# Kernel optimization log

Hardware: AMD Instinct MI355X
Metric: run time of the kernel (lower is better)

## Reference

```python
import jax, jax.numpy as jnp
import numpy as np

N = 100_000   # nodes
E = 1_600_000 # edges
F = 16        # input node features
H = 32        # embedding_size
B = 256       # graphs in batch


def setup_inputs() -> dict:
    key = jax.random.key(0)
    ks = jax.random.split(key, 13)
    s = 0.1  # small init scale for weights
    return {
        "x": jax.random.normal(ks[0], (N, F), jnp.float32),
        "edge_index": jax.random.randint(ks[1], (2, E), 0, N, dtype=jnp.int64),
        "batch_index": jnp.sort(jax.random.randint(ks[2], (N,), 0, B, dtype=jnp.int64)),
        "W0": jax.random.normal(ks[3], (F, H), jnp.float32) * s,
        "b0": jax.random.normal(ks[4], (H,), jnp.float32) * s,
        "W1": jax.random.normal(ks[5], (H, H), jnp.float32) * s,
        "b1": jax.random.normal(ks[6], (H,), jnp.float32) * s,
        "W2": jax.random.normal(ks[7], (H, H), jnp.float32) * s,
        "b2": jax.random.normal(ks[8], (H,), jnp.float32) * s,
        "W3": jax.random.normal(ks[9], (H, H), jnp.float32) * s,
        "b3": jax.random.normal(ks[10], (H, H), jnp.float32)[:, 0] * s,
        "W_out": jax.random.normal(ks[11], (3 * H, 1), jnp.float32) * s,
        "b_out": jax.random.normal(ks[12], (1,), jnp.float32) * s,
    }


def _gcn_forward(x, edge_index, batch_index,
                 W0, b0, W1, b1, W2, b2, W3, b3, W_out, b_out):
    src, dst = edge_index[0], edge_index[1]
    n = x.shape[0]
    # GCN symmetric normalization with self-loops: deg includes the +1 self-loop
    deg = jax.ops.segment_sum(jnp.ones(src.shape[0], x.dtype), dst, num_segments=n) + 1.0
    dinv = jax.lax.rsqrt(deg)
    edge_coef = (dinv[src] * dinv[dst])[:, None]   # [E,1]
    self_coef = (dinv * dinv)[:, None]             # [N,1]

    def conv(h, W, b):
        # x' = D^{-1/2}(A+I)D^{-1/2} (h W) + b  (PyG GCNConv)
        hW = h @ W
        agg = jax.ops.segment_sum(hW[src] * edge_coef, dst, num_segments=n)
        agg = agg + hW * self_coef  # self-loop contribution
        return agg + b

    h = jnp.tanh(conv(x, W0, b0))
    h = jnp.tanh(conv(h, W1, b1))
    h = jnp.tanh(conv(h, W2, b2))
    h = jnp.tanh(conv(h, W3, b3))

    # Global max / mean / add pooling over batch_index
    gmax = jax.ops.segment_max(h, batch_index, num_segments=B)
    gsum = jax.ops.segment_sum(h, batch_index, num_segments=B)
    cnt = jax.ops.segment_sum(jnp.ones(n, h.dtype), batch_index, num_segments=B)
    gmean = gsum / jnp.maximum(cnt, 1.0)[:, None]
    pooled = jnp.concatenate([gmax, gmean, gsum], axis=1)  # [B, 3H]

    out = pooled @ W_out + b_out  # [B, 1]
    return out, pooled


def reference(x, edge_index, batch_index,
              W0, b0, W1, b1, W2, b2, W3, b3, W_out, b_out):
    return _gcn_forward(x, edge_index, batch_index,
                        W0, b0, W1, b1, W2, b2, W3, b3, W_out, b_out)
```

## Files before the change

### kernel.cpp

```cpp
#include <hip/hip_runtime.h>
#include <math.h>

#define N_NODES 100000
#define N_EDGES 1600000
#define F_IN    16
#define H_DIM   32
#define B_GRAPHS 256

#define BSHIFT  7
#define BSIZE   128
#define NBUCKET ((N_NODES + BSIZE - 1) / BSIZE)
#define EPB     8192
#define NCHUNK  ((N_EDGES + EPB - 1) / EPB)
#define CAPB    2560
#define CSTRIDE 2944
#define TPAD    (NBUCKET * CSTRIDE)
#define NPB     16
#define LAYER_BLOCKS (N_NODES / NPB)

__device__ inline float bf_lo(unsigned u) { return __uint_as_float(u << 16); }
__device__ inline float bf_hi(unsigned u) { return __uint_as_float(u & 0xffff0000u); }
__device__ inline unsigned pack_bf16x2(float a, float b) {
    unsigned ua = __float_as_uint(a), ub = __float_as_uint(b);
    ua += 0x7fffu + ((ua >> 16) & 1u);
    ub += 0x7fffu + ((ub >> 16) & 1u);
    return (ua >> 16) | (ub & 0xffff0000u);
}

__global__ __launch_bounds__(256) void init_cur_kernel(int* __restrict__ bucket_cur) {
    int b = blockIdx.x * 256 + threadIdx.x;
    if (b < NBUCKET) bucket_cur[b] = b * CAPB;
}

__global__ __launch_bounds__(256) void passB_kernel(const int* __restrict__ ei,
                                                    int* __restrict__ bucket_cur,
                                                    unsigned* __restrict__ rec_out) {
    __shared__ int hist[NBUCKET];
    __shared__ int gcur[NBUCKET];
    int t = threadIdx.x;
    for (int k = t; k < NBUCKET; k += 256) hist[k] = 0;
    __syncthreads();

    const int* dst = ei + N_EDGES;
    int base = blockIdx.x * EPB;
    int end  = base + EPB; if (end > N_EDGES) end = N_EDGES;

    for (int e = base + t; e < end; e += 256) atomicAdd(&hist[dst[e] >> BSHIFT], 1);
    __syncthreads();

    for (int k = t; k < NBUCKET; k += 256) {
        int h = hist[k];
        gcur[k] = h ? atomicAdd(&bucket_cur[k], h) : 0;
    }
    __syncthreads();

    for (int e = base + t; e < end; e += 256) {
        int d = dst[e], s = ei[e];
        int bk = d >> BSHIFT;
        int pos = atomicAdd(&gcur[bk], 1);
        rec_out[pos] = (unsigned)s | ((unsigned)(d & (BSIZE - 1)) << 20);
    }
}

__global__ __launch_bounds__(256) void dinv_kernel(const unsigned* __restrict__ rec,
                                                   const int* __restrict__ bucket_end,
                                                   float* __restrict__ dinv) {
    __shared__ int cnt[BSIZE];
    int t = threadIdx.x, b = blockIdx.x;
    if (t < BSIZE) cnt[t] = 0;
    __syncthreads();
    int e1 = bucket_end[b];
    for (int e = b * CAPB + t; e < e1; e += 256) atomicAdd(&cnt[rec[e] >> 20], 1);
    __syncthreads();
    int nd = (b << BSHIFT) + t;
    if (t < BSIZE && nd < N_NODES) dinv[nd] = rsqrtf((float)cnt[t] + 1.0f);
}

__global__ __launch_bounds__(256) void passC_kernel(const unsigned* __restrict__ rec,
                                                    const int* __restrict__ bucket_end,
                                                    const float* __restrict__ dinv,
                                                    int2* __restrict__ row_meta,
                                                    int2* __restrict__ csr) {
    __shared__ unsigned stage[CAPB];
    __shared__ int cnt[BSIZE];
    __shared__ int pds[BSIZE];
    __shared__ int cur[BSIZE];
    __shared__ float sdv[BSIZE];
    int t = threadIdx.x, b = blockIdx.x;
    int node0 = b << BSHIFT;
    int e0 = b * CAPB;
    int n = bucket_end[b] - e0;
    int pbase = b * CSTRIDE;
    if (t < BSIZE) {
        cnt[t] = 0;
        int nd = node0 + t;
        sdv[t] = (nd < N_NODES) ? dinv[nd] : 0.f;
    }
    __syncthreads();
    for (int k = t; k < n; k += 256) {
        unsigned r = rec[e0 + k];
        stage[k] = r;
        atomicAdd(&cnt[r >> 20], 1);
    }
    __syncthreads();
    int pd = 0;
    if (t < BSIZE) { pd = (cnt[t] + 3) & ~3; pds[t] = pd; }
    __syncthreads();
    for (int off = 1; off < BSIZE; off <<= 1) {
        int v = (t < BSIZE && t >= off) ? pds[t - off] : 0;
        __syncthreads();
        if (t < BSIZE) pds[t] += v;
        __syncthreads();
    }
    if (t < BSIZE) {
        int startp = pbase + pds[t] - pd;
        cur[t] = startp;
        int nd = node0 + t;
        if (nd < N_NODES) {
            row_meta[nd] = make_int2(startp, pd);
            for (int k = startp + cnt[t]; k < startp + pd; ++k)
                csr[k] = make_int2(nd, 0);
        }
    }
    __syncthreads();
    for (int k = t; k < n; k += 256) {
        unsigned r = stage[k];
        int dl = r >> 20;
        int s  = r & 0xFFFFF;
        int pos = atomicAdd(&cur[dl], 1);
        csr[pos] = make_int2(s, __float_as_int(dinv[s] * sdv[dl]));
    }
}

template <int FIN, bool PACKED>
__global__ __launch_bounds__(256) void layer_kernel(
        const void* __restrict__ h_in_v,
        const int2* __restrict__ row_meta,
        const int4* __restrict__ csr4,
        const float* __restrict__ dinv,
        const float* __restrict__ W,
        const float* __restrict__ bias,
        unsigned* __restrict__ h_out) {
    constexpr int STR = FIN + 1;
    __shared__ float sW[FIN * H_DIM];
    __shared__ float sb[H_DIM];
    __shared__ float agg[NPB][STR];
    int t = threadIdx.x;
    for (int k = t; k < FIN * H_DIM; k += 256) sW[k] = W[k];
    if (t < H_DIM) sb[t] = bias[t];

    int nl = t >> 4, ln = t & 15;
    int i = blockIdx.x * NPB + nl;
    int2 m = row_meta[i];
    float di = dinv[i], di2 = di * di;
    int q    = m.x >> 1;
    int qend = (m.x + m.y) >> 1;

    if (PACKED) {
        const unsigned* hp = (const unsigned*)h_in_v;
        unsigned u = hp[i * 16 + ln];
        float acc0 = bf_lo(u) * di2, acc1 = bf_hi(u) * di2;
        for (; q + 4 <= qend; q += 4) {
            int4 a = csr4[q], b = csr4[q + 1], c = csr4[q + 2], d = csr4[q + 3];
            unsigned v0 = hp[a.x * 16 + ln], v1 = hp[a.z * 16 + ln];
            unsigned v2 = hp[b.x * 16 + ln], v3 = hp[b.z * 16 + ln];
            unsigned v4 = hp[c.x * 16 + ln], v5 = hp[c.z * 16 + ln];
            unsigned v6 = hp[d.x * 16 + ln], v7 = hp[d.z * 16 + ln];
            float c0 = __int_as_float(a.y), c1 = __int_as_float(a.w);
            float c2 = __int_as_float(b.y), c3 = __int_as_float(b.w);
            float c4 = __int_as_float(c.y), c5 = __int_as_float(c.w);
            float c6 = __int_as_float(d.y), c7 = __int_as_float(d.w);
            acc0 += bf_lo(v0) * c0 + bf_lo(v1) * c1 + bf_lo(v2) * c2 + bf_lo(v3) * c3
                  + bf_lo(v4) * c4 + bf_lo(v5) * c5 + bf_lo(v6) * c6 + bf_lo(v7) * c7;
            acc1 += bf_hi(v0) * c0 + bf_hi(v1) * c1 + bf_hi(v2) * c2 + bf_hi(v3) * c3
                  + bf_hi(v4) * c4 + bf_hi(v5) * c5 + bf_hi(v6) * c6 + bf_hi(v7) * c7;
        }
        if (q < qend) {
            int4 a = csr4[q], b = csr4[q + 1];
            unsigned v0 = hp[a.x * 16 + ln], v1 = hp[a.z * 16 + ln];
            unsigned v2 = hp[b.x * 16 + ln], v3 = hp[b.z * 16 + ln];
            float c0 = __int_as_float(a.y), c1 = __int_as_float(a.w);
            float c2 = __int_as_float(b.y), c3 = __int_as_float(b.w);
            acc0 += bf_lo(v0) * c0 + bf_lo(v1) * c1 + bf_lo(v2) * c2 + bf_lo(v3) * c3;
            acc1 += bf_hi(v0) * c0 + bf_hi(v1) * c1 + bf_hi(v2) * c2 + bf_hi(v3) * c3;
        }
        agg[nl][2 * ln]     = acc0;
        agg[nl][2 * ln + 1] = acc1;
    } else {
        const float* xf = (const float*)h_in_v;
        float acc = xf[i * F_IN + ln] * di2;
        for (; q + 4 <= qend; q += 4) {
            int4 a = csr4[q], b = csr4[q + 1], c = csr4[q + 2], d = csr4[q + 3];
            float v0 = xf[a.x * F_IN + ln], v1 = xf[a.z * F_IN + ln];
            float v2 = xf[b.x * F_IN + ln], v3 = xf[b.z * F_IN + ln];
            float v4 = xf[c.x * F_IN + ln], v5 = xf[c.z * F_IN + ln];
            float v6 = xf[d.x * F_IN + ln], v7 = xf[d.z * F_IN + ln];
            acc += v0 * __int_as_float(a.y) + v1 * __int_as_float(a.w)
                 + v2 * __int_as_float(b.y) + v3 * __int_as_float(b.w)
                 + v4 * __int_as_float(c.y) + v5 * __int_as_float(c.w)
                 + v6 * __int_as_float(d.y) + v7 * __int_as_float(d.w);
        }
        if (q < qend) {
            int4 a = csr4[q], b = csr4[q + 1];
            float v0 = xf[a.x * F_IN + ln], v1 = xf[a.z * F_IN + ln];
            float v2 = xf[b.x * F_IN + ln], v3 = xf[b.z * F_IN + ln];
            acc += v0 * __int_as_float(a.y) + v1 * __int_as_float(a.w)
                 + v2 * __int_as_float(b.y) + v3 * __int_as_float(b.w);
        }
        agg[nl][ln] = acc;
    }
    __syncthreads();

    int j0 = 2 * ln;
    float o0 = sb[j0], o1 = sb[j0 + 1];
    const float* arow = &agg[nl][0];
#pragma unroll
    for (int k = 0; k < FIN; ++k) {
        float a = arow[k];
        o0 += a * sW[k * H_DIM + j0];
        o1 += a * sW[k * H_DIM + j0 + 1];
    }
    h_out[i * 16 + ln] = pack_bf16x2(tanhf(o0), tanhf(o1));
}

__global__ __launch_bounds__(256) void pool_kernel(const unsigned* __restrict__ hp,
                                                   const int* __restrict__ batch,
                                                   const float* __restrict__ Wout,
                                                   const float* __restrict__ bout,
                                                   float* __restrict__ out) {
    int b = blockIdx.x;
    int t = threadIdx.x;
    int lane_n = t >> 5;
    int j = t & 31;

    int lo = 0, hi = N_NODES;
    while (lo < hi) { int mid = (lo + hi) >> 1; if (batch[mid] < b) lo = mid + 1; else hi = mid; }
    int start = lo;
    hi = N_NODES;
    while (lo < hi) { int mid = (lo + hi) >> 1; if (batch[mid] < b + 1) lo = mid + 1; else hi = mid; }
    int end = lo;

    float vmax = -INFINITY, vsum = 0.f;
    for (int i = start + lane_n; i < end; i += 8) {
        unsigned q = hp[i * 16 + (j >> 1)];
        float v = (j & 1) ? bf_hi(q) : bf_lo(q);
        vmax = fmaxf(vmax, v);
        vsum += v;
    }

    __shared__ float smax[8][32];
    __shared__ float ssum[8][32];
    __shared__ float pool96[96];
    smax[lane_n][j] = vmax;
    ssum[lane_n][j] = vsum;
    __syncthreads();

    if (t < 32) {
        float m = smax[0][t], s = ssum[0][t];
#pragma unroll
        for (int n = 1; n < 8; ++n) { m = fmaxf(m, smax[n][t]); s += ssum[n][t]; }
        int cnt = end - start;
        float mean = s / fmaxf((float)cnt, 1.0f);
        pool96[t]      = m;
        pool96[32 + t] = mean;
        pool96[64 + t] = s;
    }
    __syncthreads();

    if (t < 96) out[B_GRAPHS + b * 96 + t] = pool96[t];

    __shared__ float dotbuf[96];
    if (t < 96) dotbuf[t] = pool96[t] * Wout[t];
    __syncthreads();
    if (t == 0) {
        float acc = 0.f;
#pragma unroll
        for (int k = 0; k < 96; ++k) acc += dotbuf[k];
        out[b] = acc + bout[0];
    }
}

extern "C" void kernel_launch(void* const* d_in, const int* in_sizes, int n_in,
                              void* d_out, int out_size, void* d_ws, size_t ws_size,
                              hipStream_t stream) {
    const float* x     = (const float*)d_in[0];
    const int*   ei    = (const int*)  d_in[1];
    const int*   batch = (const int*)  d_in[2];
    const float* W0    = (const float*)d_in[3];
    const float* b0    = (const float*)d_in[4];
    const float* W1    = (const float*)d_in[5];
    const float* b1    = (const float*)d_in[6];
    const float* W2    = (const float*)d_in[7];
    const float* b2    = (const float*)d_in[8];
    const float* W3    = (const float*)d_in[9];
    const float* b3    = (const float*)d_in[10];
    const float* Wout  = (const float*)d_in[11];
    const float* bout  = (const float*)d_in[12];
    float* out = (float*)d_out;

    char* p = (char*)d_ws;
    float*    dinv       = (float*)p;    p += (size_t)N_NODES * 4;
    unsigned* hA         = (unsigned*)p; p += (size_t)N_NODES * 16 * 4;
    unsigned* rec        = (unsigned*)p; p += (size_t)NBUCKET * CAPB * 4;
    int2*     csr        = (int2*)p;     p += (size_t)TPAD * 8;
    int2*     row_meta   = (int2*)p;     p += (size_t)N_NODES * 8;
    int*      bucket_cur = (int*)p;      p += NBUCKET * 4;
    unsigned* hB = rec;

    init_cur_kernel<<<(NBUCKET + 255) / 256, 256, 0, stream>>>(bucket_cur);
    passB_kernel<<<NCHUNK, 256, 0, stream>>>(ei, bucket_cur, rec);
    dinv_kernel<<<NBUCKET, 256, 0, stream>>>(rec, bucket_cur, dinv);
    passC_kernel<<<NBUCKET, 256, 0, stream>>>(rec, bucket_cur, dinv, row_meta, csr);

    layer_kernel<F_IN, false><<<LAYER_BLOCKS, 256, 0, stream>>>(
        x,  row_meta, (const int4*)csr, dinv, W0, b0, hA);
    layer_kernel<H_DIM, true><<<LAYER_BLOCKS, 256, 0, stream>>>(
        hA, row_meta, (const int4*)csr, dinv, W1, b1, hB);
    layer_kernel<H_DIM, true><<<LAYER_BLOCKS, 256, 0, stream>>>(
        hB, row_meta, (const int4*)csr, dinv, W2, b2, hA);
    layer_kernel<H_DIM, true><<<LAYER_BLOCKS, 256, 0, stream>>>(
        hA, row_meta, (const int4*)csr, dinv, W3, b3, hB);

    pool_kernel<<<B_GRAPHS, 256, 0, stream>>>(hB, batch, Wout, bout, out);
}
```

Before: 265.5 us.

## Sort nodes by degree within buckets and use nontemporal CSR loads

Inside each 128-node bucket, passC now bitonic-sorts nodes by padded degree and writes a perm array with row metadata in sorted order. The layer kernels read nodes through this permutation, so the 16 nodes sharing a block have similar edge counts and waves are less imbalanced. Streaming loads of rec and csr are marked nontemporal to keep them from evicting the gathered feature rows. The cost is an extra sort and scan in passC, plus one more indirection per node in every layer.

```diff
diff --git a/kernel.cpp b/kernel.cpp
--- a/kernel.cpp
+++ b/kernel.cpp
@@ -18,6 +18,8 @@
 #define NPB     16
 #define LAYER_BLOCKS (N_NODES / NPB)
 
+typedef int v4i __attribute__((ext_vector_type(4)));
+
 __device__ inline float bf_lo(unsigned u) { return __uint_as_float(u << 16); }
 __device__ inline float bf_hi(unsigned u) { return __uint_as_float(u & 0xffff0000u); }
 __device__ inline unsigned pack_bf16x2(float a, float b) {
@@ -70,7 +72,8 @@
     if (t < BSIZE) cnt[t] = 0;
     __syncthreads();
     int e1 = bucket_end[b];
-    for (int e = b * CAPB + t; e < e1; e += 256) atomicAdd(&cnt[rec[e] >> 20], 1);
+    for (int e = b * CAPB + t; e < e1; e += 256)
+        atomicAdd(&cnt[__builtin_nontemporal_load(&rec[e]) >> 20], 1);
     __syncthreads();
     int nd = (b << BSHIFT) + t;
     if (t < BSIZE && nd < N_NODES) dinv[nd] = rsqrtf((float)cnt[t] + 1.0f);
@@ -80,9 +83,11 @@
                                                     const int* __restrict__ bucket_end,
                                                     const float* __restrict__ dinv,
                                                     int2* __restrict__ row_meta,
+                                                    int* __restrict__ perm,
                                                     int2* __restrict__ csr) {
     __shared__ unsigned stage[CAPB];
     __shared__ int cnt[BSIZE];
+    __shared__ unsigned key[BSIZE];
     __shared__ int pds[BSIZE];
     __shared__ int cur[BSIZE];
     __shared__ float sdv[BSIZE];
@@ -98,13 +103,34 @@
     }
     __syncthreads();
     for (int k = t; k < n; k += 256) {
-        unsigned r = rec[e0 + k];
+        unsigned r = __builtin_nontemporal_load(&rec[e0 + k]);
         stage[k] = r;
         atomicAdd(&cnt[r >> 20], 1);
     }
     __syncthreads();
-    int pd = 0;
-    if (t < BSIZE) { pd = (cnt[t] + 3) & ~3; pds[t] = pd; }
+
+    if (t < BSIZE) {
+        int pd = (cnt[t] + 3) & ~3;
+        unsigned valid = (node0 + t < N_NODES) ? 1u : 0u;
+        key[t] = (valid << 30) | ((unsigned)pd << 16) | (unsigned)t;
+    }
+    __syncthreads();
+    for (unsigned kk = 2; kk <= BSIZE; kk <<= 1) {
+        for (unsigned jj = kk >> 1; jj > 0; jj >>= 1) {
+            if (t < BSIZE) {
+                unsigned ixj = t ^ jj;
+                if (ixj > (unsigned)t) {
+                    unsigned a = key[t], c = key[ixj];
+                    bool up = ((t & kk) == 0);
+                    if (up ? (a < c) : (a > c)) { key[t] = c; key[ixj] = a; }
+                }
+            }
+            __syncthreads();
+        }
+    }
+
+    int pd_r = 0;
+    if (t < BSIZE) { pd_r = (int)((key[t] >> 16) & 0x3FFFu); pds[t] = pd_r; }
     __syncthreads();
     for (int off = 1; off < BSIZE; off <<= 1) {
         int v = (t < BSIZE && t >= off) ? pds[t - off] : 0;
@@ -113,13 +139,16 @@
         __syncthreads();
     }
     if (t < BSIZE) {
-        int startp = pbase + pds[t] - pd;
-        cur[t] = startp;
-        int nd = node0 + t;
-        if (nd < N_NODES) {
-            row_meta[nd] = make_int2(startp, pd);
-            for (int k = startp + cnt[t]; k < startp + pd; ++k)
-                csr[k] = make_int2(nd, 0);
+        unsigned k = key[t];
+        int ln = (int)(k & 0x7Fu);
+        int startp = pbase + pds[t] - pd_r;
+        cur[ln] = startp;
+        if ((k >> 30) & 1u) {
+            int nd = node0 + ln;
+            row_meta[node0 + t] = make_int2(startp, pd_r);
+            perm[node0 + t]     = nd;
+            for (int q = startp + cnt[ln]; q < startp + pd_r; ++q)
+                csr[q] = make_int2(nd, 0);
         }
     }
     __syncthreads();
@@ -136,7 +165,8 @@
 __global__ __launch_bounds__(256) void layer_kernel(
         const void* __restrict__ h_in_v,
         const int2* __restrict__ row_meta,
-        const int4* __restrict__ csr4,
+        const int* __restrict__ perm,
+        const v4i* __restrict__ csr4,
         const float* __restrict__ dinv,
         const float* __restrict__ W,
         const float* __restrict__ bias,
@@ -150,8 +180,9 @@
     if (t < H_DIM) sb[t] = bias[t];
 
     int nl = t >> 4, ln = t & 15;
-    int i = blockIdx.x * NPB + nl;
-    int2 m = row_meta[i];
+    int ri = blockIdx.x * NPB + nl;
+    int i = perm[ri];
+    int2 m = row_meta[ri];
     float di = dinv[i], di2 = di * di;
     int q    = m.x >> 1;
     int qend = (m.x + m.y) >> 1;
@@ -161,7 +192,10 @@
         unsigned u = hp[i * 16 + ln];
         float acc0 = bf_lo(u) * di2, acc1 = bf_hi(u) * di2;
         for (; q + 4 <= qend; q += 4) {
-            int4 a = csr4[q], b = csr4[q + 1], c = csr4[q + 2], d = csr4[q + 3];
+            v4i a = __builtin_nontemporal_load(&csr4[q]);
+            v4i b = __builtin_nontemporal_load(&csr4[q + 1]);
+            v4i c = __builtin_nontemporal_load(&csr4[q + 2]);
+            v4i d = __builtin_nontemporal_load(&csr4[q + 3]);
             unsigned v0 = hp[a.x * 16 + ln], v1 = hp[a.z * 16 + ln];
             unsigned v2 = hp[b.x * 16 + ln], v3 = hp[b.z * 16 + ln];
             unsigned v4 = hp[c.x * 16 + ln], v5 = hp[c.z * 16 + ln];
@@ -176,7 +210,8 @@
                   + bf_hi(v4) * c4 + bf_hi(v5) * c5 + bf_hi(v6) * c6 + bf_hi(v7) * c7;
         }
         if (q < qend) {
-            int4 a = csr4[q], b = csr4[q + 1];
+            v4i a = __builtin_nontemporal_load(&csr4[q]);
+            v4i b = __builtin_nontemporal_load(&csr4[q + 1]);
             unsigned v0 = hp[a.x * 16 + ln], v1 = hp[a.z * 16 + ln];
             unsigned v2 = hp[b.x * 16 + ln], v3 = hp[b.z * 16 + ln];
             float c0 = __int_as_float(a.y), c1 = __int_as_float(a.w);
@@ -190,7 +225,10 @@
         const float* xf = (const float*)h_in_v;
         float acc = xf[i * F_IN + ln] * di2;
         for (; q + 4 <= qend; q += 4) {
-            int4 a = csr4[q], b = csr4[q + 1], c = csr4[q + 2], d = csr4[q + 3];
+            v4i a = __builtin_nontemporal_load(&csr4[q]);
+            v4i b = __builtin_nontemporal_load(&csr4[q + 1]);
+            v4i c = __builtin_nontemporal_load(&csr4[q + 2]);
+            v4i d = __builtin_nontemporal_load(&csr4[q + 3]);
             float v0 = xf[a.x * F_IN + ln], v1 = xf[a.z * F_IN + ln];
             float v2 = xf[b.x * F_IN + ln], v3 = xf[b.z * F_IN + ln];
             float v4 = xf[c.x * F_IN + ln], v5 = xf[c.z * F_IN + ln];
@@ -201,7 +239,8 @@
                  + v6 * __int_as_float(d.y) + v7 * __int_as_float(d.w);
         }
         if (q < qend) {
-            int4 a = csr4[q], b = csr4[q + 1];
+            v4i a = __builtin_nontemporal_load(&csr4[q]);
+            v4i b = __builtin_nontemporal_load(&csr4[q + 1]);
             float v0 = xf[a.x * F_IN + ln], v1 = xf[a.z * F_IN + ln];
             float v2 = xf[b.x * F_IN + ln], v3 = xf[b.z * F_IN + ln];
             acc += v0 * __int_as_float(a.y) + v1 * __int_as_float(a.w)
@@ -303,23 +342,25 @@
     unsigned* hA         = (unsigned*)p; p += (size_t)N_NODES * 16 * 4;
     unsigned* rec        = (unsigned*)p; p += (size_t)NBUCKET * CAPB * 4;
     int2*     csr        = (int2*)p;     p += (size_t)TPAD * 8;
-    int2*     row_meta   = (int2*)p;     p += (size_t)N_NODES * 8;
+    int2*     row_meta   = (int2*)p;     p += (size_t)NBUCKET * BSIZE * 8;
+    int*      perm       = (int*)p;      p += (size_t)NBUCKET * BSIZE * 4;
     int*      bucket_cur = (int*)p;      p += NBUCKET * 4;
     unsigned* hB = rec;
 
     init_cur_kernel<<<(NBUCKET + 255) / 256, 256, 0, stream>>>(bucket_cur);
     passB_kernel<<<NCHUNK, 256, 0, stream>>>(ei, bucket_cur, rec);
     dinv_kernel<<<NBUCKET, 256, 0, stream>>>(rec, bucket_cur, dinv);
-    passC_kernel<<<NBUCKET, 256, 0, stream>>>(rec, bucket_cur, dinv, row_meta, csr);
+    passC_kernel<<<NBUCKET, 256, 0, stream>>>(rec, bucket_cur, dinv,
+                                              row_meta, perm, csr);
 
     layer_kernel<F_IN, false><<<LAYER_BLOCKS, 256, 0, stream>>>(
-        x,  row_meta, (const int4*)csr, dinv, W0, b0, hA);
+        x,  row_meta, perm, (const v4i*)csr, dinv, W0, b0, hA);
     layer_kernel<H_DIM, true><<<LAYER_BLOCKS, 256, 0, stream>>>(
-        hA, row_meta, (const int4*)csr, dinv, W1, b1, hB);
+        hA, row_meta, perm, (const v4i*)csr, dinv, W1, b1, hB);
     layer_kernel<H_DIM, true><<<LAYER_BLOCKS, 256, 0, stream>>>(
-        hB, row_meta, (const int4*)csr, dinv, W2, b2, hA);
+        hB, row_meta, perm, (const v4i*)csr, dinv, W2, b2, hA);
     layer_kernel<H_DIM, true><<<LAYER_BLOCKS, 256, 0, stream>>>(
-        hA, row_meta, (const int4*)csr, dinv, W3, b3, hB);
+        hA, row_meta, perm, (const v4i*)csr, dinv, W3, b3, hB);
 
     pool_kernel<<<B_GRAPHS, 256, 0, stream>>>(hB, batch, Wout, bout, out);
 }
```

Result: slower. 315.5 us (+18.8%).
